# Performance work log

Measured on AMD Instinct MI355X. Metric: run time of the kernel, lower is better.

Reference implementation:

```python
import jax, jax.numpy as jnp
import numpy as np

D = 256
N_EDGES = 8192
N_CORNERS = 4096


def setup_inputs() -> dict:
    key = jax.random.key(0)
    ks = jax.random.split(key, 8)
    scale = 1.0 / np.sqrt(D)
    return {
        "edge_pred": jax.random.uniform(ks[0], (N_EDGES,), dtype=jnp.float32),
        "edge_corner": jax.random.randint(ks[1], (N_EDGES, 2), 0, N_CORNERS, dtype=jnp.int64),
        "all_corners": jax.random.uniform(ks[2], (N_CORNERS, 2), dtype=jnp.float32),
        "edge_x": jax.random.normal(ks[3], (N_EDGES, D), dtype=jnp.float32),
        "image_x": jax.random.normal(ks[4], (1024,), dtype=jnp.float32),
        "W1": jax.random.normal(ks[5], (D, D), dtype=jnp.float32) * scale,
        "b1": jnp.zeros((D,), dtype=jnp.float32),
        "W2": jax.random.normal(ks[6], (D, D), dtype=jnp.float32) * scale,
        "b2": jnp.zeros((D,), dtype=jnp.float32),
        "W3": jax.random.normal(ks[7], (3 * D, D), dtype=jnp.float32) * scale,
        "b3": jnp.zeros((D,), dtype=jnp.float32),
    }


def _linear_block(x, W, b):
    # LinearBlock: Linear followed by ReLU
    return jax.nn.relu(x @ W + b)


def reference(edge_pred, edge_corner, all_corners, edge_x, image_x, W1, b1, W2, b2, W3, b3):
    # 'fully' branch of MPModule.forward. edge_pred/edge_corner/all_corners/image_x
    # are unused in this branch (kept for signature fidelity).
    e1 = _linear_block(edge_x, W1, b1)              # [N, D]
    # (e1.unsqueeze(1) * e1).mean(-1) == (e1 @ e1.T) / D   -> [N, N]
    sim1 = (e1 @ e1.T) / D
    e2 = _linear_block(edge_x, W2, b2)
    sim2 = (e2 @ e2.T) / D
    # (edge_x * sim.unsqueeze(-1)).sum(1) == sim @ edge_x  -> [N, D]
    agg1 = sim1 @ edge_x
    agg2 = sim2 @ edge_x
    cat = jnp.concatenate([edge_x, agg1, agg2], axis=-1)  # [N, 3D]
    out = _linear_block(cat, W3, b3)                      # [N, D]
    return out
```

## Files before the change

### kernel.cpp

```cpp
#include <hip/hip_runtime.h>

#define NE 8192
#define DD 256
#define NSPLIT 16

typedef __attribute__((ext_vector_type(8))) short short8;
typedef __attribute__((ext_vector_type(4))) short short4v;
typedef __attribute__((ext_vector_type(8))) __bf16 bf16x8;
typedef __attribute__((ext_vector_type(4))) float floatx4;

__device__ __forceinline__ unsigned short f2bf(float f) {
  union { float f; unsigned int i; } v; v.f = f;
  unsigned int r = v.i + 0x7fffu + ((v.i >> 16) & 1u);
  return (unsigned short)(r >> 16);
}

__device__ __forceinline__ floatx4 mfma_bf16(short8 a, short8 b, floatx4 c) {
  return __builtin_amdgcn_mfma_f32_16x16x32_bf16(
      __builtin_bit_cast(bf16x8, a), __builtin_bit_cast(bf16x8, b), c, 0, 0, 0);
}

__device__ __forceinline__ void tcvt_tile(float* ls,
                                          const float* __restrict__ src, int C,
                                          unsigned short* __restrict__ dst, int R,
                                          int r0, int c0, int tid) {
  const int rr = tid >> 4, c4 = (tid & 15) * 4;
#pragma unroll
  for (int k = 0; k < 4; ++k)
    *(floatx4*)&ls[(rr + k * 16) * 68 + c4] =
        *(const floatx4*)&src[(size_t)(r0 + rr + k * 16) * C + c0 + c4];
  __syncthreads();
  const int cc = tid >> 2, rb = (tid & 3) * 16;
  short8 o0, o1;
#pragma unroll
  for (int i = 0; i < 8; ++i) {
    o0[i] = (short)f2bf(ls[(rb + i) * 68 + cc]);
    o1[i] = (short)f2bf(ls[(rb + 8 + i) * 68 + cc]);
  }
  unsigned short* dp = &dst[(size_t)(c0 + cc) * R + r0 + rb];
  *(short8*)dp = o0;
  *(short8*)(dp + 8) = o1;
}

__global__ void cvt_all(const float* __restrict__ x, unsigned short* __restrict__ xb,
                        unsigned short* __restrict__ xT,
                        const float* __restrict__ W1, unsigned short* __restrict__ W1t,
                        const float* __restrict__ W2, unsigned short* __restrict__ W2t,
                        const float* __restrict__ W3, unsigned short* __restrict__ W3t0) {
  __shared__ float ls[64 * 68];
  const int b = blockIdx.x, tid = threadIdx.x;
  if (b < 512) {
    const int r0 = (b >> 2) * 64, c0 = (b & 3) * 64;
    const int rr = tid >> 4, c4 = (tid & 15) * 4;
#pragma unroll
    for (int k = 0; k < 4; ++k) {
      floatx4 v = *(const floatx4*)&x[(size_t)(r0 + rr + k * 16) * DD + c0 + c4];
      *(floatx4*)&ls[(rr + k * 16) * 68 + c4] = v;
      short4v s;
#pragma unroll
      for (int c = 0; c < 4; ++c) s[c] = (short)f2bf(v[c]);
      *(short4v*)&xb[(size_t)(r0 + rr + k * 16) * DD + c0 + c4] = s;
    }
    __syncthreads();
    const int cc = tid >> 2, rb = (tid & 3) * 16;
    short8 o0, o1;
#pragma unroll
    for (int i = 0; i < 8; ++i) {
      o0[i] = (short)f2bf(ls[(rb + i) * 68 + cc]);
      o1[i] = (short)f2bf(ls[(rb + 8 + i) * 68 + cc]);
    }
    unsigned short* dp = &xT[(size_t)(c0 + cc) * NE + r0 + rb];
    *(short8*)dp = o0;
    *(short8*)(dp + 8) = o1;
  } else {
    int t = b - 512;
    const float* src = (t < 16) ? W1 : ((t < 32) ? W2 : W3);
    unsigned short* dst = (t < 16) ? W1t : ((t < 32) ? W2t : W3t0);
    t &= 15;
    tcvt_tile(ls, src, DD, dst, DD, (t >> 2) * 64, (t & 3) * 64, tid);
  }
}

__global__ __launch_bounds__(256, 3)
void e_gemm(const unsigned short* __restrict__ xb,
            const unsigned short* __restrict__ W1t, const float* __restrict__ b1,
            const unsigned short* __restrict__ W2t, const float* __restrict__ b2,
            unsigned short* __restrict__ e1, unsigned short* __restrict__ e2,
            unsigned short* __restrict__ e1T, unsigned short* __restrict__ e2T)
{
  __shared__ __align__(16) unsigned short smA[64 * 136];
  __shared__ __align__(16) unsigned short smB1[64 * 136];
  __shared__ __align__(16) unsigned short smB2[64 * 136];
  const int T = threadIdx.x, lane = T & 63, wv = T >> 6;
  const int q = lane >> 4, r = lane & 15;
  const int col0 = blockIdx.x * 64, row0 = blockIdx.y * 64;

  floatx4 acc1[4], acc2[4];
#pragma unroll
  for (int j = 0; j < 4; ++j) {
    acc1[j] = (floatx4){0.f, 0.f, 0.f, 0.f};
    acc2[j] = (floatx4){0.f, 0.f, 0.f, 0.f};
  }

  short8 pa[4], pb1[4], pb2[4];
#pragma unroll
  for (int p = 0; p < 4; ++p) {
    const int id = p * 256 + T, rr = id >> 4, k8 = (id & 15) * 8;
    pa[p]  = *(const short8*)&xb[(size_t)(row0 + rr) * DD + k8];
    pb1[p] = *(const short8*)&W1t[(size_t)(col0 + rr) * DD + k8];
    pb2[p] = *(const short8*)&W2t[(size_t)(col0 + rr) * DD + k8];
  }

  for (int kc = 0; kc < 256; kc += 128) {
#pragma unroll
    for (int p = 0; p < 4; ++p) {
      const int id = p * 256 + T, rr = id >> 4, k8 = (id & 15) * 8;
      *(short8*)&smA[rr * 136 + k8]  = pa[p];
      *(short8*)&smB1[rr * 136 + k8] = pb1[p];
      *(short8*)&smB2[rr * 136 + k8] = pb2[p];
    }
    __syncthreads();
    if (kc + 128 < 256) {
#pragma unroll
      for (int p = 0; p < 4; ++p) {
        const int id = p * 256 + T, rr = id >> 4, k8 = (id & 15) * 8;
        pa[p]  = *(const short8*)&xb[(size_t)(row0 + rr) * DD + kc + 128 + k8];
        pb1[p] = *(const short8*)&W1t[(size_t)(col0 + rr) * DD + kc + 128 + k8];
        pb2[p] = *(const short8*)&W2t[(size_t)(col0 + rr) * DD + kc + 128 + k8];
      }
    }
#pragma unroll
    for (int ks = 0; ks < 4; ++ks) {
      short8 af = *(const short8*)&smA[(wv * 16 + r) * 136 + ks * 32 + q * 8];
#pragma unroll
      for (int j = 0; j < 4; ++j) {
        short8 b1f = *(const short8*)&smB1[(j * 16 + r) * 136 + ks * 32 + q * 8];
        short8 b2f = *(const short8*)&smB2[(j * 16 + r) * 136 + ks * 32 + q * 8];
        acc1[j] = mfma_bf16(af, b1f, acc1[j]);
        acc2[j] = mfma_bf16(af, b2f, acc2[j]);
      }
    }
    __syncthreads();
  }

#pragma unroll
  for (int j = 0; j < 4; ++j) {
    const int col = col0 + j * 16 + r;
    const int rowb = row0 + wv * 16 + q * 4;
    const float b1v = b1[col], b2v = b2[col];
    short4v t1, t2;
#pragma unroll
    for (int t = 0; t < 4; ++t) {
      unsigned short h1 = f2bf(fmaxf(acc1[j][t] + b1v, 0.0f));
      unsigned short h2 = f2bf(fmaxf(acc2[j][t] + b2v, 0.0f));
      t1[t] = (short)h1; t2[t] = (short)h2;
      e1[(size_t)(rowb + t) * DD + col] = h1;
      e2[(size_t)(rowb + t) * DD + col] = h2;
    }
    *(short4v*)&e1T[(size_t)col * NE + rowb] = t1;
    *(short4v*)&e2T[(size_t)col * NE + rowb] = t2;
  }
}

__global__ __launch_bounds__(256, 4)
void atb(const unsigned short* __restrict__ e1T, const unsigned short* __restrict__ e2T,
         const unsigned short* __restrict__ xT, float* __restrict__ P_T)
{
  __shared__ __align__(16) unsigned short smA[64 * 136];
  __shared__ __align__(16) unsigned short smB[64 * 136];
  const int T = threadIdx.x, lane = T & 63, wv = T >> 6;
  const int q = lane >> 4, r = lane & 15;
  const int m0 = (blockIdx.x >> 2) * 64, n0 = (blockIdx.x & 3) * 64;
  const int y = blockIdx.y, z = blockIdx.z;
  const int j0 = y * (NE / NSPLIT);
  const unsigned short* E = z ? e2T : e1T;
  float* P = P_T + (size_t)(z * NSPLIT + y) * 65536;

  floatx4 acc[4];
#pragma unroll
  for (int j = 0; j < 4; ++j) acc[j] = (floatx4){0.f, 0.f, 0.f, 0.f};

  short8 pa[4], pb[4];
#pragma unroll
  for (int p = 0; p < 4; ++p) {
    const int id = p * 256 + T, mm = id >> 4, j8 = (id & 15) * 8;
    pa[p] = *(const short8*)&E[(size_t)(m0 + mm) * NE + j0 + j8];
    pb[p] = *(const short8*)&xT[(size_t)(n0 + mm) * NE + j0 + j8];
  }

  for (int jc = 0; jc < NE / NSPLIT; jc += 128) {
#pragma unroll
    for (int p = 0; p < 4; ++p) {
      const int id = p * 256 + T, mm = id >> 4, j8 = (id & 15) * 8;
      *(short8*)&smA[mm * 136 + j8] = pa[p];
      *(short8*)&smB[mm * 136 + j8] = pb[p];
    }
    __syncthreads();
    if (jc + 128 < NE / NSPLIT) {
#pragma unroll
      for (int p = 0; p < 4; ++p) {
        const int id = p * 256 + T, mm = id >> 4, j8 = (id & 15) * 8;
        pa[p] = *(const short8*)&E[(size_t)(m0 + mm) * NE + j0 + jc + 128 + j8];
        pb[p] = *(const short8*)&xT[(size_t)(n0 + mm) * NE + j0 + jc + 128 + j8];
      }
    }
#pragma unroll
    for (int ks = 0; ks < 4; ++ks) {
      short8 af = *(const short8*)&smA[(wv * 16 + r) * 136 + ks * 32 + q * 8];
#pragma unroll
      for (int j = 0; j < 4; ++j) {
        short8 bf = *(const short8*)&smB[(j * 16 + r) * 136 + ks * 32 + q * 8];
        acc[j] = mfma_bf16(af, bf, acc[j]);
      }
    }
    __syncthreads();
  }
#pragma unroll
  for (int j = 0; j < 4; ++j) {
    const int n = n0 + j * 16 + r;
    const int m = m0 + wv * 16 + q * 4;
    *(floatx4*)&P[(size_t)n * DD + m] = acc[j];
  }
}

__global__ void reduce_g(const float* __restrict__ P_T, float* __restrict__ G_T) {
  int idx = blockIdx.x * 256 + threadIdx.x;
  int z = idx >> 14, off = idx & 16383;
  const floatx4* Pp = (const floatx4*)P_T;
  floatx4 s = (floatx4){0.f, 0.f, 0.f, 0.f};
#pragma unroll
  for (int y = 0; y < NSPLIT; ++y)
    s += Pp[(size_t)(z * NSPLIT + y) * 16384 + off];
  ((floatx4*)G_T)[idx] = s;
}

__global__ __launch_bounds__(256, 2)
void h_mfma(const float* __restrict__ G_T, const float* __restrict__ W3,
            unsigned short* __restrict__ H1t, unsigned short* __restrict__ H2t)
{
  __shared__ __align__(16) unsigned short smA[64 * 136];
  __shared__ __align__(16) unsigned short smB[64 * 136];
  const int T = threadIdx.x, lane = T & 63, wv = T >> 6;
  const int q = lane >> 4, r = lane & 15;
  const int z = blockIdx.z;
  const int me0 = (blockIdx.x >> 2) * 64, m30 = (blockIdx.x & 3) * 64;
  const float* G = G_T + (size_t)z * 65536;
  unsigned short* Ht = z ? H2t : H1t;
  const int woff = 256 + z * 256;

  floatx4 acc[4];
#pragma unroll
  for (int j = 0; j < 4; ++j) acc[j] = (floatx4){0.f, 0.f, 0.f, 0.f};

  for (int lc = 0; lc < 256; lc += 128) {
#pragma unroll
    for (int p = 0; p < 2; ++p) {
      const int id = p * 256 + T, lb = id >> 4, e4 = id & 15;
      floatx4 grow[4], wrow[4];
#pragma unroll
      for (int i = 0; i < 4; ++i) {
        grow[i] = *(const floatx4*)&G[(size_t)(lc + lb * 4 + i) * DD + me0 + e4 * 4];
        wrow[i] = *(const floatx4*)&W3[(size_t)(woff + lc + lb * 4 + i) * DD + m30 + e4 * 4];
      }
#pragma unroll
      for (int s4 = 0; s4 < 4; ++s4) {
        const int c = (s4 + e4) & 3;
        short4v ga = {(short)f2bf(grow[0][c] * 0.00390625f),
                      (short)f2bf(grow[1][c] * 0.00390625f),
                      (short)f2bf(grow[2][c] * 0.00390625f),
                      (short)f2bf(grow[3][c] * 0.00390625f)};
        short4v wa = {(short)f2bf(wrow[0][c]), (short)f2bf(wrow[1][c]),
                      (short)f2bf(wrow[2][c]), (short)f2bf(wrow[3][c])};
        *(short4v*)&smA[(e4 * 4 + c) * 136 + lb * 4] = ga;
        *(short4v*)&smB[(e4 * 4 + c) * 136 + lb * 4] = wa;
      }
    }
    __syncthreads();
#pragma unroll
    for (int ks = 0; ks < 4; ++ks) {
      short8 af = *(const short8*)&smA[(wv * 16 + r) * 136 + ks * 32 + q * 8];
#pragma unroll
      for (int j = 0; j < 4; ++j) {
        short8 bf = *(const short8*)&smB[(j * 16 + r) * 136 + ks * 32 + q * 8];
        acc[j] = mfma_bf16(af, bf, acc[j]);
      }
    }
    __syncthreads();
  }
#pragma unroll
  for (int j = 0; j < 4; ++j) {
    const int m3 = m30 + j * 16 + r;
    const int me = me0 + wv * 16 + q * 4;
    short4v v;
#pragma unroll
    for (int i = 0; i < 4; ++i) v[i] = (short)f2bf(acc[j][i]);
    *(short4v*)&Ht[(size_t)m3 * DD + me] = v;
  }
}

__global__ __launch_bounds__(256, 4)
void out_gemm(const unsigned short* __restrict__ xb,
              const unsigned short* __restrict__ e1, const unsigned short* __restrict__ e2,
              const unsigned short* __restrict__ W3t0,
              const unsigned short* __restrict__ H1t, const unsigned short* __restrict__ H2t,
              const float* __restrict__ b3, float* __restrict__ out)
{
  __shared__ __align__(16) unsigned short smA[64 * 136];
  __shared__ __align__(16) unsigned short smB[64 * 136];
  const int T = threadIdx.x, lane = T & 63, wv = T >> 6;
  const int q = lane >> 4, r = lane & 15;
  const int col0 = blockIdx.x * 64, row0 = blockIdx.y * 64;

  const unsigned short* As[3] = {xb, e1, e2};
  const unsigned short* Bs[3] = {W3t0, H1t, H2t};

  floatx4 acc[4];
#pragma unroll
  for (int j = 0; j < 4; ++j) acc[j] = (floatx4){0.f, 0.f, 0.f, 0.f};

  short8 qa[4], qb[4];
#pragma unroll
  for (int p = 0; p < 4; ++p) {
    const int id = p * 256 + T, rr = id >> 4, k8 = (id & 15) * 8;
    qa[p] = *(const short8*)&As[0][(size_t)(row0 + rr) * DD + k8];
    qb[p] = *(const short8*)&Bs[0][(size_t)(col0 + rr) * DD + k8];
  }

  for (int rd = 0; rd < 6; ++rd) {
#pragma unroll
    for (int p = 0; p < 4; ++p) {
      const int id = p * 256 + T, rr = id >> 4, k8 = (id & 15) * 8;
      *(short8*)&smA[rr * 136 + k8] = qa[p];
      *(short8*)&smB[rr * 136 + k8] = qb[p];
    }
    __syncthreads();
    if (rd + 1 < 6) {
      const int s = (rd + 1) >> 1, kc = ((rd + 1) & 1) * 128;
      const unsigned short* A = As[s];
      const unsigned short* B = Bs[s];
#pragma unroll
      for (int p = 0; p < 4; ++p) {
        const int id = p * 256 + T, rr = id >> 4, k8 = (id & 15) * 8;
        qa[p] = *(const short8*)&A[(size_t)(row0 + rr) * DD + kc + k8];
        qb[p] = *(const short8*)&B[(size_t)(col0 + rr) * DD + kc + k8];
      }
    }
#pragma unroll
    for (int ks = 0; ks < 4; ++ks) {
      short8 af = *(const short8*)&smA[(wv * 16 + r) * 136 + ks * 32 + q * 8];
#pragma unroll
      for (int j = 0; j < 4; ++j) {
        short8 bf = *(const short8*)&smB[(j * 16 + r) * 136 + ks * 32 + q * 8];
        acc[j] = mfma_bf16(af, bf, acc[j]);
      }
    }
    __syncthreads();
  }
#pragma unroll
  for (int j = 0; j < 4; ++j) {
    const int col = col0 + j * 16 + r;
    const float bv = b3[col];
    const int rowb = row0 + wv * 16 + q * 4;
#pragma unroll
    for (int t = 0; t < 4; ++t)
      out[(size_t)(rowb + t) * DD + col] = fmaxf(acc[j][t] + bv, 0.0f);
  }
}

extern "C" void kernel_launch(void* const* d_in, const int* in_sizes, int n_in,
                              void* d_out, int out_size, void* d_ws, size_t ws_size,
                              hipStream_t stream) {
  (void)in_sizes; (void)n_in; (void)out_size; (void)ws_size;
  const float* x  = (const float*)d_in[3];
  const float* W1 = (const float*)d_in[5];
  const float* b1 = (const float*)d_in[6];
  const float* W2 = (const float*)d_in[7];
  const float* b2 = (const float*)d_in[8];
  const float* W3 = (const float*)d_in[9];
  const float* b3 = (const float*)d_in[10];
  float* out = (float*)d_out;

  char* ws = (char*)d_ws;
  const size_t MB = 1u << 20;
  const size_t KB = 1u << 10;
  unsigned short* xb   = (unsigned short*)ws;
  unsigned short* xT   = (unsigned short*)(ws + 4 * MB);
  unsigned short* e1   = (unsigned short*)(ws + 8 * MB);
  unsigned short* e2   = (unsigned short*)(ws + 12 * MB);
  unsigned short* e1T  = (unsigned short*)(ws + 16 * MB);
  unsigned short* e2T  = (unsigned short*)(ws + 20 * MB);
  unsigned short* W1t  = (unsigned short*)(ws + 24 * MB);
  unsigned short* W2t  = (unsigned short*)(ws + 24 * MB + 128 * KB);
  unsigned short* W3t0 = (unsigned short*)(ws + 24 * MB + 256 * KB);
  unsigned short* H1t  = (unsigned short*)(ws + 24 * MB + 384 * KB);
  unsigned short* H2t  = (unsigned short*)(ws + 24 * MB + 512 * KB);
  float* G_T           = (float*)(ws + 24 * MB + 640 * KB);
  float* P_T           = (float*)(ws + 25 * MB);

  cvt_all<<<560, 256, 0, stream>>>(x, xb, xT, W1, W1t, W2, W2t, W3, W3t0);
  e_gemm<<<dim3(4, 128), 256, 0, stream>>>(xb, W1t, b1, W2t, b2, e1, e2, e1T, e2T);
  atb<<<dim3(16, NSPLIT, 2), 256, 0, stream>>>(e1T, e2T, xT, P_T);
  reduce_g<<<128, 256, 0, stream>>>(P_T, G_T);
  h_mfma<<<dim3(16, 1, 2), 256, 0, stream>>>(G_T, W3, H1t, H2t);
  out_gemm<<<dim3(4, 128), 256, 0, stream>>>(xb, e1, e2, W3t0, H1t, H2t, b3, out);
}
```

Before: 122.1 us.

## Retile GEMM kernels to 128x64 tiles with 2x4 MFMA per wave

```diff
diff --git a/kernel.cpp b/kernel.cpp
--- a/kernel.cpp
+++ b/kernel.cpp
@@ -2,7 +2,7 @@
 
 #define NE 8192
 #define DD 256
-#define NSPLIT 16
+#define NSPLIT 32
 
 typedef __attribute__((ext_vector_type(8))) short short8;
 typedef __attribute__((ext_vector_type(4))) short short4v;
@@ -81,64 +81,80 @@
   }
 }
 
-__global__ __launch_bounds__(256, 3)
+__global__ __launch_bounds__(256, 2)
 void e_gemm(const unsigned short* __restrict__ xb,
             const unsigned short* __restrict__ W1t, const float* __restrict__ b1,
             const unsigned short* __restrict__ W2t, const float* __restrict__ b2,
             unsigned short* __restrict__ e1, unsigned short* __restrict__ e2,
             unsigned short* __restrict__ e1T, unsigned short* __restrict__ e2T)
 {
-  __shared__ __align__(16) unsigned short smA[64 * 136];
-  __shared__ __align__(16) unsigned short smB1[64 * 136];
-  __shared__ __align__(16) unsigned short smB2[64 * 136];
+  __shared__ __align__(16) unsigned short smA[128 * 72];
+  __shared__ __align__(16) unsigned short smB[64 * 72];
   const int T = threadIdx.x, lane = T & 63, wv = T >> 6;
   const int q = lane >> 4, r = lane & 15;
-  const int col0 = blockIdx.x * 64, row0 = blockIdx.y * 64;
-
-  floatx4 acc1[4], acc2[4];
-#pragma unroll
-  for (int j = 0; j < 4; ++j) {
-    acc1[j] = (floatx4){0.f, 0.f, 0.f, 0.f};
-    acc2[j] = (floatx4){0.f, 0.f, 0.f, 0.f};
-  }
-
-  short8 pa[4], pb1[4], pb2[4];
+  const int col0 = blockIdx.x * 64, row0 = blockIdx.y * 128;
+  const int z = blockIdx.z;
+  const unsigned short* Wt = z ? W2t : W1t;
+  const float* bi = z ? b2 : b1;
+  unsigned short* eo = z ? e2 : e1;
+  unsigned short* eoT = z ? e2T : e1T;
+
+  floatx4 acc[2][4];
+#pragma unroll
+  for (int i = 0; i < 2; ++i)
+#pragma unroll
+    for (int j = 0; j < 4; ++j) acc[i][j] = (floatx4){0.f, 0.f, 0.f, 0.f};
+
+  short8 pa[4], pb[2];
 #pragma unroll
   for (int p = 0; p < 4; ++p) {
-    const int id = p * 256 + T, rr = id >> 4, k8 = (id & 15) * 8;
-    pa[p]  = *(const short8*)&xb[(size_t)(row0 + rr) * DD + k8];
-    pb1[p] = *(const short8*)&W1t[(size_t)(col0 + rr) * DD + k8];
-    pb2[p] = *(const short8*)&W2t[(size_t)(col0 + rr) * DD + k8];
-  }
-
-  for (int kc = 0; kc < 256; kc += 128) {
+    const int id = p * 256 + T, rr = id >> 3, k8 = (id & 7) * 8;
+    pa[p] = *(const short8*)&xb[(size_t)(row0 + rr) * DD + k8];
+  }
+#pragma unroll
+  for (int p = 0; p < 2; ++p) {
+    const int id = p * 256 + T, nn = id >> 3, k8 = (id & 7) * 8;
+    pb[p] = *(const short8*)&Wt[(size_t)(col0 + nn) * DD + k8];
+  }
+
+  for (int kc = 0; kc < 256; kc += 64) {
 #pragma unroll
     for (int p = 0; p < 4; ++p) {
-      const int id = p * 256 + T, rr = id >> 4, k8 = (id & 15) * 8;
-      *(short8*)&smA[rr * 136 + k8]  = pa[p];
-      *(short8*)&smB1[rr * 136 + k8] = pb1[p];
-      *(short8*)&smB2[rr * 136 + k8] = pb2[p];
-    }
-    __syncthreads();
-    if (kc + 128 < 256) {
+      const int id = p * 256 + T, rr = id >> 3, k8 = (id & 7) * 8;
+      *(short8*)&smA[rr * 72 + k8] = pa[p];
+    }
+#pragma unroll
+    for (int p = 0; p < 2; ++p) {
+      const int id = p * 256 + T, nn = id >> 3, k8 = (id & 7) * 8;
+      *(short8*)&smB[nn * 72 + k8] = pb[p];
+    }
+    __syncthreads();
+    if (kc + 64 < 256) {
 #pragma unroll
       for (int p = 0; p < 4; ++p) {
-        const int id = p * 256 + T, rr = id >> 4, k8 = (id & 15) * 8;
-        pa[p]  = *(const short8*)&xb[(size_t)(row0 + rr) * DD + kc + 128 + k8];
-        pb1[p] = *(const short8*)&W1t[(size_t)(col0 + rr) * DD + kc + 128 + k8];
-        pb2[p] = *(const short8*)&W2t[(size_t)(col0 + rr) * DD + kc + 128 + k8];
-      }
-    }
-#pragma unroll
-    for (int ks = 0; ks < 4; ++ks) {
-      short8 af = *(const short8*)&smA[(wv * 16 + r) * 136 + ks * 32 + q * 8];
-#pragma unroll
-      for (int j = 0; j < 4; ++j) {
-        short8 b1f = *(const short8*)&smB1[(j * 16 + r) * 136 + ks * 32 + q * 8];
-        short8 b2f = *(const short8*)&smB2[(j * 16 + r) * 136 + ks * 32 + q * 8];
-        acc1[j] = mfma_bf16(af, b1f, acc1[j]);
-        acc2[j] = mfma_bf16(af, b2f, acc2[j]);
-      }
+        const int id = p * 256 + T, rr = id >> 3, k8 = (id & 7) * 8;
+        pa[p] = *(const short8*)&xb[(size_t)(row0 + rr) * DD + kc + 64 + k8];
+      }
+#pragma unroll
+      for (int p = 0; p < 2; ++p) {
+        const int id = p * 256 + T, nn = id >> 3, k8 = (id & 7) * 8;
+        pb[p] = *(const short8*)&Wt[(size_t)(col0 + nn) * DD + kc + 64 + k8];
+      }
+    }
+#pragma unroll
+    for (int ks = 0; ks < 2; ++ks) {
+      short8 af[2], bf[4];
+#pragma unroll
+      for (int i = 0; i < 2; ++i)
+        af[i] = *(const short8*)&smA[(wv * 32 + i * 16 + r) * 72 + ks * 32 + q * 8];
+#pragma unroll
+      for (int j = 0; j < 4; ++j)
+        bf[j] = *(const short8*)&smB[(j * 16 + r) * 72 + ks * 32 + q * 8];
+#pragma unroll
+      for (int i = 0; i < 2; ++i)
+#pragma unroll
+        for (int j = 0; j < 4; ++j)
+          acc[i][j] = mfma_bf16(af[i], bf[j], acc[i][j]);
     }
     __syncthreads();
   }
@@ -146,81 +162,103 @@
 #pragma unroll
   for (int j = 0; j < 4; ++j) {
     const int col = col0 + j * 16 + r;
-    const int rowb = row0 + wv * 16 + q * 4;
-    const float b1v = b1[col], b2v = b2[col];
-    short4v t1, t2;
-#pragma unroll
-    for (int t = 0; t < 4; ++t) {
-      unsigned short h1 = f2bf(fmaxf(acc1[j][t] + b1v, 0.0f));
-      unsigned short h2 = f2bf(fmaxf(acc2[j][t] + b2v, 0.0f));
-      t1[t] = (short)h1; t2[t] = (short)h2;
-      e1[(size_t)(rowb + t) * DD + col] = h1;
-      e2[(size_t)(rowb + t) * DD + col] = h2;
-    }
-    *(short4v*)&e1T[(size_t)col * NE + rowb] = t1;
-    *(short4v*)&e2T[(size_t)col * NE + rowb] = t2;
-  }
-}
-
-__global__ __launch_bounds__(256, 4)
+    const float bv = bi[col];
+#pragma unroll
+    for (int i = 0; i < 2; ++i) {
+      const int rowb = row0 + wv * 32 + i * 16 + q * 4;
+      short4v tv;
+#pragma unroll
+      for (int t = 0; t < 4; ++t) {
+        unsigned short h = f2bf(fmaxf(acc[i][j][t] + bv, 0.0f));
+        tv[t] = (short)h;
+        eo[(size_t)(rowb + t) * DD + col] = h;
+      }
+      *(short4v*)&eoT[(size_t)col * NE + rowb] = tv;
+    }
+  }
+}
+
+__global__ __launch_bounds__(256, 2)
 void atb(const unsigned short* __restrict__ e1T, const unsigned short* __restrict__ e2T,
          const unsigned short* __restrict__ xT, float* __restrict__ P_T)
 {
-  __shared__ __align__(16) unsigned short smA[64 * 136];
-  __shared__ __align__(16) unsigned short smB[64 * 136];
+  __shared__ __align__(16) unsigned short smA[128 * 72];
+  __shared__ __align__(16) unsigned short smB[64 * 72];
   const int T = threadIdx.x, lane = T & 63, wv = T >> 6;
   const int q = lane >> 4, r = lane & 15;
-  const int m0 = (blockIdx.x >> 2) * 64, n0 = (blockIdx.x & 3) * 64;
+  const int m0 = (blockIdx.x >> 2) * 128, n0 = (blockIdx.x & 3) * 64;
   const int y = blockIdx.y, z = blockIdx.z;
   const int j0 = y * (NE / NSPLIT);
   const unsigned short* E = z ? e2T : e1T;
   float* P = P_T + (size_t)(z * NSPLIT + y) * 65536;
 
-  floatx4 acc[4];
-#pragma unroll
-  for (int j = 0; j < 4; ++j) acc[j] = (floatx4){0.f, 0.f, 0.f, 0.f};
-
-  short8 pa[4], pb[4];
+  floatx4 acc[2][4];
+#pragma unroll
+  for (int i = 0; i < 2; ++i)
+#pragma unroll
+    for (int j = 0; j < 4; ++j) acc[i][j] = (floatx4){0.f, 0.f, 0.f, 0.f};
+
+  short8 pa[4], pb[2];
 #pragma unroll
   for (int p = 0; p < 4; ++p) {
-    const int id = p * 256 + T, mm = id >> 4, j8 = (id & 15) * 8;
+    const int id = p * 256 + T, mm = id >> 3, j8 = (id & 7) * 8;
     pa[p] = *(const short8*)&E[(size_t)(m0 + mm) * NE + j0 + j8];
-    pb[p] = *(const short8*)&xT[(size_t)(n0 + mm) * NE + j0 + j8];
-  }
-
-  for (int jc = 0; jc < NE / NSPLIT; jc += 128) {
+  }
+#pragma unroll
+  for (int p = 0; p < 2; ++p) {
+    const int id = p * 256 + T, nn = id >> 3, j8 = (id & 7) * 8;
+    pb[p] = *(const short8*)&xT[(size_t)(n0 + nn) * NE + j0 + j8];
+  }
+
+  for (int jc = 0; jc < NE / NSPLIT; jc += 64) {
 #pragma unroll
     for (int p = 0; p < 4; ++p) {
-      const int id = p * 256 + T, mm = id >> 4, j8 = (id & 15) * 8;
-      *(short8*)&smA[mm * 136 + j8] = pa[p];
-      *(short8*)&smB[mm * 136 + j8] = pb[p];
-    }
-    __syncthreads();
-    if (jc + 128 < NE / NSPLIT) {
+      const int id = p * 256 + T, mm = id >> 3, j8 = (id & 7) * 8;
+      *(short8*)&smA[mm * 72 + j8] = pa[p];
+    }
+#pragma unroll
+    for (int p = 0; p < 2; ++p) {
+      const int id = p * 256 + T, nn = id >> 3, j8 = (id & 7) * 8;
+      *(short8*)&smB[nn * 72 + j8] = pb[p];
+    }
+    __syncthreads();
+    if (jc + 64 < NE / NSPLIT) {
 #pragma unroll
       for (int p = 0; p < 4; ++p) {
-        const int id = p * 256 + T, mm = id >> 4, j8 = (id & 15) * 8;
-        pa[p] = *(const short8*)&E[(size_t)(m0 + mm) * NE + j0 + jc + 128 + j8];
-        pb[p] = *(const short8*)&xT[(size_t)(n0 + mm) * NE + j0 + jc + 128 + j8];
-      }
-    }
-#pragma unroll
-    for (int ks = 0; ks < 4; ++ks) {
-      short8 af = *(const short8*)&smA[(wv * 16 + r) * 136 + ks * 32 + q * 8];
-#pragma unroll
-      for (int j = 0; j < 4; ++j) {
-        short8 bf = *(const short8*)&smB[(j * 16 + r) * 136 + ks * 32 + q * 8];
-        acc[j] = mfma_bf16(af, bf, acc[j]);
-      }
-    }
-    __syncthreads();
-  }
-#pragma unroll
-  for (int j = 0; j < 4; ++j) {
-    const int n = n0 + j * 16 + r;
-    const int m = m0 + wv * 16 + q * 4;
-    *(floatx4*)&P[(size_t)n * DD + m] = acc[j];
-  }
+        const int id = p * 256 + T, mm = id >> 3, j8 = (id & 7) * 8;
+        pa[p] = *(const short8*)&E[(size_t)(m0 + mm) * NE + j0 + jc + 64 + j8];
+      }
+#pragma unroll
+      for (int p = 0; p < 2; ++p) {
+        const int id = p * 256 + T, nn = id >> 3, j8 = (id & 7) * 8;
+        pb[p] = *(const short8*)&xT[(size_t)(n0 + nn) * NE + j0 + jc + 64 + j8];
+      }
+    }
+#pragma unroll
+    for (int ks = 0; ks < 2; ++ks) {
+      short8 af[2], bf[4];
+#pragma unroll
+      for (int i = 0; i < 2; ++i)
+        af[i] = *(const short8*)&smA[(wv * 32 + i * 16 + r) * 72 + ks * 32 + q * 8];
+#pragma unroll
+      for (int j = 0; j < 4; ++j)
+        bf[j] = *(const short8*)&smB[(j * 16 + r) * 72 + ks * 32 + q * 8];
+#pragma unroll
+      for (int i = 0; i < 2; ++i)
+#pragma unroll
+        for (int j = 0; j < 4; ++j)
+          acc[i][j] = mfma_bf16(af[i], bf[j], acc[i][j]);
+    }
+    __syncthreads();
+  }
+#pragma unroll
+  for (int i = 0; i < 2; ++i)
+#pragma unroll
+    for (int j = 0; j < 4; ++j) {
+      const int n = n0 + j * 16 + r;
+      const int m = m0 + wv * 32 + i * 16 + q * 4;
+      *(floatx4*)&P[(size_t)n * DD + m] = acc[i][j];
+    }
 }
 
 __global__ void reduce_g(const float* __restrict__ P_T, float* __restrict__ G_T) {
@@ -298,61 +336,81 @@
   }
 }
 
-__global__ __launch_bounds__(256, 4)
+__global__ __launch_bounds__(256, 2)
 void out_gemm(const unsigned short* __restrict__ xb,
               const unsigned short* __restrict__ e1, const unsigned short* __restrict__ e2,
               const unsigned short* __restrict__ W3t0,
               const unsigned short* __restrict__ H1t, const unsigned short* __restrict__ H2t,
               const float* __restrict__ b3, float* __restrict__ out)
 {
-  __shared__ __align__(16) unsigned short smA[64 * 136];
-  __shared__ __align__(16) unsigned short smB[64 * 136];
+  __shared__ __align__(16) unsigned short smA[128 * 72];
+  __shared__ __align__(16) unsigned short smB[64 * 72];
   const int T = threadIdx.x, lane = T & 63, wv = T >> 6;
   const int q = lane >> 4, r = lane & 15;
-  const int col0 = blockIdx.x * 64, row0 = blockIdx.y * 64;
+  const int col0 = blockIdx.x * 64, row0 = blockIdx.y * 128;
 
   const unsigned short* As[3] = {xb, e1, e2};
   const unsigned short* Bs[3] = {W3t0, H1t, H2t};
 
-  floatx4 acc[4];
-#pragma unroll
-  for (int j = 0; j < 4; ++j) acc[j] = (floatx4){0.f, 0.f, 0.f, 0.f};
-
-  short8 qa[4], qb[4];
+  floatx4 acc[2][4];
+#pragma unroll
+  for (int i = 0; i < 2; ++i)
+#pragma unroll
+    for (int j = 0; j < 4; ++j) acc[i][j] = (floatx4){0.f, 0.f, 0.f, 0.f};
+
+  short8 pa[4], pb[2];
 #pragma unroll
   for (int p = 0; p < 4; ++p) {
-    const int id = p * 256 + T, rr = id >> 4, k8 = (id & 15) * 8;
-    qa[p] = *(const short8*)&As[0][(size_t)(row0 + rr) * DD + k8];
-    qb[p] = *(const short8*)&Bs[0][(size_t)(col0 + rr) * DD + k8];
-  }
-
-  for (int rd = 0; rd < 6; ++rd) {
+    const int id = p * 256 + T, rr = id >> 3, k8 = (id & 7) * 8;
+    pa[p] = *(const short8*)&As[0][(size_t)(row0 + rr) * DD + k8];
+  }
+#pragma unroll
+  for (int p = 0; p < 2; ++p) {
+    const int id = p * 256 + T, nn = id >> 3, k8 = (id & 7) * 8;
+    pb[p] = *(const short8*)&Bs[0][(size_t)(col0 + nn) * DD + k8];
+  }
+
+  for (int rd = 0; rd < 12; ++rd) {
 #pragma unroll
     for (int p = 0; p < 4; ++p) {
-      const int id = p * 256 + T, rr = id >> 4, k8 = (id & 15) * 8;
-      *(short8*)&smA[rr * 136 + k8] = qa[p];
-      *(short8*)&smB[rr * 136 + k8] = qb[p];
-    }
-    __syncthreads();
-    if (rd + 1 < 6) {
-      const int s = (rd + 1) >> 1, kc = ((rd + 1) & 1) * 128;
+      const int id = p * 256 + T, rr = id >> 3, k8 = (id & 7) * 8;
+      *(short8*)&smA[rr * 72 + k8] = pa[p];
+    }
+#pragma unroll
+    for (int p = 0; p < 2; ++p) {
+      const int id = p * 256 + T, nn = id >> 3, k8 = (id & 7) * 8;
+      *(short8*)&smB[nn * 72 + k8] = pb[p];
+    }
+    __syncthreads();
+    if (rd + 1 < 12) {
+      const int s = (rd + 1) >> 2, kc = ((rd + 1) & 3) * 64;
       const unsigned short* A = As[s];
       const unsigned short* B = Bs[s];
 #pragma unroll
       for (int p = 0; p < 4; ++p) {
-        const int id = p * 256 + T, rr = id >> 4, k8 = (id & 15) * 8;
-        qa[p] = *(const short8*)&A[(size_t)(row0 + rr) * DD + kc + k8];
-        qb[p] = *(const short8*)&B[(size_t)(col0 + rr) * DD + kc + k8];
-      }
-    }
-#pragma unroll
-    for (int ks = 0; ks < 4; ++ks) {
-      short8 af = *(const short8*)&smA[(wv * 16 + r) * 136 + ks * 32 + q * 8];
-#pragma unroll
-      for (int j = 0; j < 4; ++j) {
-        short8 bf = *(const short8*)&smB[(j * 16 + r) * 136 + ks * 32 + q * 8];
-        acc[j] = mfma_bf16(af, bf, acc[j]);
-      }
+        const int id = p * 256 + T, rr = id >> 3, k8 = (id & 7) * 8;
+        pa[p] = *(const short8*)&A[(size_t)(row0 + rr) * DD + kc + k8];
+      }
+#pragma unroll
+      for (int p = 0; p < 2; ++p) {
+        const int id = p * 256 + T, nn = id >> 3, k8 = (id & 7) * 8;
+        pb[p] = *(const short8*)&B[(size_t)(col0 + nn) * DD + kc + k8];
+      }
+    }
+#pragma unroll
+    for (int ks = 0; ks < 2; ++ks) {
+      short8 af[2], bf[4];
+#pragma unroll
+      for (int i = 0; i < 2; ++i)
+        af[i] = *(const short8*)&smA[(wv * 32 + i * 16 + r) * 72 + ks * 32 + q * 8];
+#pragma unroll
+      for (int j = 0; j < 4; ++j)
+        bf[j] = *(const short8*)&smB[(j * 16 + r) * 72 + ks * 32 + q * 8];
+#pragma unroll
+      for (int i = 0; i < 2; ++i)
+#pragma unroll
+        for (int j = 0; j < 4; ++j)
+          acc[i][j] = mfma_bf16(af[i], bf[j], acc[i][j]);
     }
     __syncthreads();
   }
@@ -360,10 +418,13 @@
   for (int j = 0; j < 4; ++j) {
     const int col = col0 + j * 16 + r;
     const float bv = b3[col];
-    const int rowb = row0 + wv * 16 + q * 4;
-#pragma unroll
-    for (int t = 0; t < 4; ++t)
-      out[(size_t)(rowb + t) * DD + col] = fmaxf(acc[j][t] + bv, 0.0f);
+#pragma unroll
+    for (int i = 0; i < 2; ++i) {
+      const int rowb = row0 + wv * 32 + i * 16 + q * 4;
+#pragma unroll
+      for (int t = 0; t < 4; ++t)
+        out[(size_t)(rowb + t) * DD + col] = fmaxf(acc[i][j][t] + bv, 0.0f);
+    }
   }
 }
 
@@ -398,9 +459,9 @@
   float* P_T           = (float*)(ws + 25 * MB);
 
   cvt_all<<<560, 256, 0, stream>>>(x, xb, xT, W1, W1t, W2, W2t, W3, W3t0);
-  e_gemm<<<dim3(4, 128), 256, 0, stream>>>(xb, W1t, b1, W2t, b2, e1, e2, e1T, e2T);
-  atb<<<dim3(16, NSPLIT, 2), 256, 0, stream>>>(e1T, e2T, xT, P_T);
+  e_gemm<<<dim3(4, 64, 2), 256, 0, stream>>>(xb, W1t, b1, W2t, b2, e1, e2, e1T, e2T);
+  atb<<<dim3(8, NSPLIT, 2), 256, 0, stream>>>(e1T, e2T, xT, P_T);
   reduce_g<<<128, 256, 0, stream>>>(P_T, G_T);
   h_mfma<<<dim3(16, 1, 2), 256, 0, stream>>>(G_T, W3, H1t, H2t);
-  out_gemm<<<dim3(4, 128), 256, 0, stream>>>(xb, e1, e2, W3t0, H1t, H2t, b3, out);
-}
+  out_gemm<<<dim3(4, 64), 256, 0, stream>>>(xb, e1, e2, W3t0, H1t, H2t, b3, out);
+}
```

Measured after the change: 128.5 us. 1.05x slower.
